# Optimization experiments

Hardware: AMD Instinct MI355X
Metric: run time of the kernel (lower is better)

Reference implementation:

```python
import jax, jax.numpy as jnp
import numpy as np

BN_EPS = 1e-5


def setup_inputs() -> dict:
    key = jax.random.key(0)
    ks = jax.random.split(key, 5)
    B, S, n_in, H, n_out = 256, 2048, 128, 256, 128
    return {
        "X": jax.random.normal(ks[0], (B, S, n_in), dtype=jnp.float32),
        "W_ih": jax.random.normal(ks[1], (H, n_in + H), dtype=jnp.float32) * (1.0 / np.sqrt(n_in + H)),
        "b_ih": jax.random.normal(ks[2], (H,), dtype=jnp.float32) * 0.02,
        "W_ho": jax.random.normal(ks[3], (n_out, H), dtype=jnp.float32) * (1.0 / np.sqrt(H)),
        "b_ho": jax.random.normal(ks[4], (n_out,), dtype=jnp.float32) * 0.02,
        "gamma": jnp.ones((H,), dtype=jnp.float32),
        "beta": jnp.zeros((H,), dtype=jnp.float32),
    }


def reference(X, W_ih, b_ih, W_ho, b_ho, gamma, beta):
    # X: (B, S, n_in). Recurrence over S with per-step training-mode BatchNorm1d
    # (batch statistics, biased variance, eps=1e-5), exact (erf) GELU.
    B = X.shape[0]
    H = W_ih.shape[0]
    Xt = jnp.transpose(X, (1, 0, 2))  # (S, B, n_in)

    def step(h, x):
        # combined: (B, n_in + H)
        z = jnp.concatenate([x, h], axis=-1) @ W_ih.T + b_ih  # (B, H)
        mu = jnp.mean(z, axis=0)
        var = jnp.var(z, axis=0)  # biased, matches torch BN training mode
        zn = (z - mu) * jax.lax.rsqrt(var + BN_EPS) * gamma + beta
        h_new = jax.nn.gelu(zn, approximate=False)
        o = jax.nn.gelu(h_new @ W_ho.T + b_ho, approximate=False)  # (B, n_out)
        return h_new, o

    h0 = jnp.zeros((B, H), dtype=X.dtype)
    _, outs = jax.lax.scan(step, h0, Xt)  # outs: (S, B, n_out)
    return jnp.transpose(outs, (1, 0, 2))  # (B, S, n_out)
```

## Files before the change

kernel.cpp:

```cpp
#include <hip/hip_runtime.h>
#include <stdint.h>


#define S_LEN 2048
#define BATCH 256
#define NIN   128
#define HID   256
#define NOUT  128

#define NBLK  128
#define NTHR  256
#define NR    16
#define NC    32
#define NO    16

#define HXW   392
#define WHOW  264

typedef short short8  __attribute__((ext_vector_type(8)));
typedef float float4v __attribute__((ext_vector_type(4)));

#define HXHI_OFF  0
#define HXLO_OFF  (16*HXW)
#define WHI_OFF   (2*16*HXW)
#define WLO_OFF   (2*16*HXW + 32*HXW)
#define WHOHI_OFF (2*16*HXW + 2*32*HXW)
#define WHOLO_OFF (WHOHI_OFF + 16*WHOW)
#define SHORTS_TOTAL (WHOLO_OFF + 16*WHOW)
#define RED_F 1088
#define SMEM_BYTES (SHORTS_TOTAL*2 + (2*RED_F + 256 + 256 + 16)*4)


#define MFMA(a,b,c) __builtin_amdgcn_mfma_f32_16x16x32_bf16(a,b,c,0,0,0)

#define AG_ST(p, v) __hip_atomic_store((p), (v), __ATOMIC_RELAXED, __HIP_MEMORY_SCOPE_AGENT)
#define AG_LD(p)    __hip_atomic_load((p), __ATOMIC_RELAXED, __HIP_MEMORY_SCOPE_AGENT)

__device__ __forceinline__ short f2bf(float f) {
  unsigned u = __float_as_uint(f);
  unsigned r = (u + 0x7fffu + ((u >> 16) & 1u)) >> 16;
  return (short)r;
}
__device__ __forceinline__ float bf2f(short s) {
  return __uint_as_float(((unsigned)(unsigned short)s) << 16);
}
__device__ __forceinline__ float gelu_f(float x) {
  return 0.5f * x * (1.0f + erff(x * 0.70710678118654752f));
}

__device__ __forceinline__ void stage_x(const float* __restrict__ X,
                                        short* hx_hi, short* hx_lo,
                                        int r0, int t, int tid) {
  int row = tid >> 4;
  int k0  = (tid & 15) * 8;
  const float* xp = X + ((size_t)(r0 + row) * S_LEN + t) * NIN + k0;
  float4v a = *(const float4v*)xp;
  float4v b = *(const float4v*)(xp + 4);
  short8 hi, lo;
#pragma unroll
  for (int j = 0; j < 4; ++j) {
    short h1 = f2bf(a[j]); hi[j] = h1; lo[j] = f2bf(a[j] - bf2f(h1));
  }
#pragma unroll
  for (int j = 0; j < 4; ++j) {
    short h1 = f2bf(b[j]); hi[4+j] = h1; lo[4+j] = f2bf(b[j] - bf2f(h1));
  }
  *(short8*)(hx_hi + row*HXW + k0) = hi;
  *(short8*)(hx_lo + row*HXW + k0) = lo;
}

__global__ void init_flags(unsigned* flags) {
  AG_ST(flags + (size_t)threadIdx.x * 32, 0u);
}

__global__ void __launch_bounds__(NTHR, 1)
rec_kernel(const float* __restrict__ X, const float* __restrict__ W_ih,
           const float* __restrict__ W_ho, const float* __restrict__ b_ho,
           const float* __restrict__ gamma, const float* __restrict__ beta,
           float* __restrict__ out, unsigned* __restrict__ flags,
           float* __restrict__ part, float* __restrict__ zbuf)
{
  extern __shared__ char smemraw[];
  short* sh      = (short*)smemraw;
  short* hx_hi   = sh + HXHI_OFF;
  short* hx_lo   = sh + HXLO_OFF;
  short* w_hi    = sh + WHI_OFF;
  short* w_lo    = sh + WLO_OFF;
  short* who_hi  = sh + WHOHI_OFF;
  short* who_lo  = sh + WHOLO_OFF;
  float* red     = (float*)(sh + SHORTS_TOTAL);
  float* red2    = red + RED_F;
  float* sscale  = red2 + RED_F;
  float* sshift  = sscale + 256;
  float* sbho    = sshift + 256;

  const int tid   = threadIdx.x;
  const int rowg  = blockIdx.x >> 3;
  const int colg  = blockIdx.x & 7;
  const int r0    = rowg * NR;
  const int c0    = colg * NC;
  const int oc0   = colg * NO;
  const int wv    = tid >> 6;
  const int lane  = tid & 63;
  const int nn    = lane & 15;
  const int quad  = lane >> 4;
  const int sub   = wv >> 1;
  const int khalf = wv & 1;

  for (int idx = tid; idx < NC * 384; idx += NTHR) {
    int r = idx / 384, j = idx % 384;
    float w = W_ih[(size_t)(c0 + r) * 384 + j];
    short hi = f2bf(w);
    w_hi[r*HXW + j] = hi;
    w_lo[r*HXW + j] = f2bf(w - bf2f(hi));
  }
  for (int idx = tid; idx < NO * 256; idx += NTHR) {
    int r = idx / 256, j = idx % 256;
    float w = W_ho[(size_t)(oc0 + r) * 256 + j];
    short hi = f2bf(w);
    who_hi[r*WHOW + j] = hi;
    who_lo[r*WHOW + j] = f2bf(w - bf2f(hi));
  }
  if (tid < NO) sbho[tid] = b_ho[oc0 + tid];
  for (int idx = tid; idx < 16 * 33; idx += NTHR) {
    int row = idx / 33, k0 = 128 + (idx % 33) * 8;
    short8 z8 = {0,0,0,0,0,0,0,0};
    *(short8*)(hx_hi + row*HXW + k0) = z8;
    *(short8*)(hx_lo + row*HXW + k0) = z8;
  }
  stage_x(X, hx_hi, hx_lo, r0, 0, tid);

  const float g_gamma = gamma[tid];
  const float g_beta  = beta[tid];
  __syncthreads();

  for (int t = 0; t < S_LEN; ++t) {
    const int p = t & 1;
    float* partp = part + p * (16 * 512);
    float* zbp   = zbuf + p * (BATCH * HID);

    float4v acc = {0.f, 0.f, 0.f, 0.f};
    {
      const short* arow_hi = hx_hi + nn*HXW;
      const short* arow_lo = hx_lo + nn*HXW;
      const short* brow_hi = w_hi + (sub*16 + nn)*HXW;
      const short* brow_lo = w_lo + (sub*16 + nn)*HXW;
      int kb = khalf*192 + quad*8;
#pragma unroll
      for (int ks = 0; ks < 6; ++ks) {
        short8 ah = *(const short8*)(arow_hi + kb);
        short8 al = *(const short8*)(arow_lo + kb);
        short8 bh = *(const short8*)(brow_hi + kb);
        short8 bl = *(const short8*)(brow_lo + kb);
        acc = MFMA(ah, bh, acc);
        acc = MFMA(ah, bl, acc);
        acc = MFMA(al, bh, acc);
        kb += 32;
      }
    }
    if (khalf == 1) {
#pragma unroll
      for (int i = 0; i < 4; ++i) red[sub*272 + (quad*4 + i)*17 + nn] = acc[i];
    }
    __syncthreads();
    if (khalf == 0) {
#pragma unroll
      for (int i = 0; i < 4; ++i) acc[i] += red[sub*272 + (quad*4 + i)*17 + nn];
      float* zb = zbp + (size_t)(r0 + quad*4) * HID + (c0 + sub*16 + nn);
#pragma unroll
      for (int i = 0; i < 4; ++i) AG_ST(zb + i*HID, acc[i]);
      float s = acc[0] + acc[1] + acc[2] + acc[3];
      float q = acc[0]*acc[0] + acc[1]*acc[1] + acc[2]*acc[2] + acc[3]*acc[3];
      s += __shfl_down(s, 32);  q += __shfl_down(q, 32);
      s += __shfl_down(s, 16);  q += __shfl_down(q, 16);
      if (lane < 16) {
        int c = c0 + sub*16 + lane;
        unsigned long long pv = ((unsigned long long)__float_as_uint(q) << 32)
                              | (unsigned long long)__float_as_uint(s);
        AG_ST((unsigned long long*)partp + (rowg*256 + c), pv);
      }
    }
    __syncthreads();

    if (tid == 0)
      AG_ST(flags + (size_t)blockIdx.x * 32, (unsigned)(t + 1));
    if (t + 1 < S_LEN) stage_x(X, hx_hi, hx_lo, r0, t + 1, tid);
    if (tid < NBLK) {
      const unsigned* fp = flags + (size_t)tid * 32;
      while (AG_LD(fp) < (unsigned)(t + 1)) __builtin_amdgcn_s_sleep(1);
    }
    __syncthreads();

    const int zrow = tid >> 4;
    const int zcb  = (tid & 15) * 16;
    unsigned long long zt[8];
    {
      const unsigned long long* zp = (const unsigned long long*)
          (zbp + (size_t)(r0 + zrow) * HID + zcb);
#pragma unroll
      for (int j = 0; j < 8; ++j) zt[j] = AG_LD(zp + j);
    }

    {
      const unsigned long long* pp = (const unsigned long long*)partp + tid;
      unsigned long long pv[16];
#pragma unroll
      for (int rg = 0; rg < 16; ++rg) pv[rg] = AG_LD(pp + rg*256);
      float sA = 0.f, sB = 0.f;
#pragma unroll
      for (int rg = 0; rg < 16; ++rg) {
        sA += __uint_as_float((unsigned)pv[rg]);
        sB += __uint_as_float((unsigned)(pv[rg] >> 32));
      }
      float mu   = sA * (1.0f/256.0f);
      float var  = sB * (1.0f/256.0f) - mu*mu;
      float rstd = rsqrtf(var + 1e-5f);
      float g    = g_gamma * rstd;
      sscale[tid] = g;
      sshift[tid] = g_beta - mu * g;
    }
    __syncthreads();

    {
      short hb[16], lb[16];
#pragma unroll
      for (int j = 0; j < 16; ++j) {
        float z  = __uint_as_float((unsigned)(zt[j >> 1] >> ((j & 1) * 32)));
        float zn = z * sscale[zcb + j] + sshift[zcb + j];
        float h  = gelu_f(zn);
        short hh = f2bf(h);
        hb[j] = hh; lb[j] = f2bf(h - bf2f(hh));
      }
      short* dh = hx_hi + zrow*HXW + 128 + zcb;
      short* dl = hx_lo + zrow*HXW + 128 + zcb;
      *(short8*)(dh)     = *(short8*)(hb);
      *(short8*)(dh + 8) = *(short8*)(hb + 8);
      *(short8*)(dl)     = *(short8*)(lb);
      *(short8*)(dl + 8) = *(short8*)(lb + 8);
    }
    __syncthreads();

    {
      float4v oacc = {0.f, 0.f, 0.f, 0.f};
      const short* arow_hi = hx_hi + nn*HXW + 128;
      const short* arow_lo = hx_lo + nn*HXW + 128;
      const short* brow_hi = who_hi + nn*WHOW;
      const short* brow_lo = who_lo + nn*WHOW;
      int kb = wv*64 + quad*8;
#pragma unroll
      for (int ks = 0; ks < 2; ++ks) {
        short8 ah = *(const short8*)(arow_hi + kb);
        short8 al = *(const short8*)(arow_lo + kb);
        short8 bh = *(const short8*)(brow_hi + kb);
        short8 bl = *(const short8*)(brow_lo + kb);
        oacc = MFMA(ah, bh, oacc);
        oacc = MFMA(ah, bl, oacc);
        oacc = MFMA(al, bh, oacc);
        kb += 32;
      }
#pragma unroll
      for (int i = 0; i < 4; ++i) red2[wv*272 + (quad*4 + i)*17 + nn] = oacc[i];
    }
    __syncthreads();
    {
      int row = tid >> 4, col = tid & 15;
      float v = red2[0*272 + row*17 + col] + red2[1*272 + row*17 + col]
              + red2[2*272 + row*17 + col] + red2[3*272 + row*17 + col]
              + sbho[col];
      out[((size_t)(r0 + row) * S_LEN + t) * NOUT + oc0 + col] = gelu_f(v);
    }
  }
}

extern "C" void kernel_launch(void* const* d_in, const int* in_sizes, int n_in,
                              void* d_out, int out_size, void* d_ws, size_t ws_size,
                              hipStream_t stream) {
  const float* X     = (const float*)d_in[0];
  const float* W_ih  = (const float*)d_in[1];
  const float* W_ho  = (const float*)d_in[3];
  const float* b_ho  = (const float*)d_in[4];
  const float* gamma = (const float*)d_in[5];
  const float* beta  = (const float*)d_in[6];
  float* out = (float*)d_out;

  unsigned* flags = (unsigned*)d_ws;
  float* part = (float*)((char*)d_ws + 16384);
  float* zbuf = part + 2 * 16 * 512;

  init_flags<<<dim3(1), dim3(NBLK), 0, stream>>>(flags);

  hipFuncSetAttribute((const void*)rec_kernel,
                      hipFuncAttributeMaxDynamicSharedMemorySize, SMEM_BYTES);

  rec_kernel<<<dim3(NBLK), dim3(NTHR), SMEM_BYTES, stream>>>(
      X, W_ih, W_ho, b_ho, gamma, beta, out, flags, part, zbuf);
}
```

Before: 13.36 ms.

## Replace flag barrier with tagged data polling and defer output GEMM

Replaces the per-step global flag barrier with step tags packed into each 64-bit z and partial-stat word, so consumers poll the data itself instead of all 128 block flags. The output projection for step t-1 is moved into the wait window of step t to hide its latency. This doubles the size of the z and stats buffers and their traffic, and adds a spin limit that could silently use stale data if it is ever hit.

```diff
diff --git a/kernel.cpp b/kernel.cpp
--- a/kernel.cpp
+++ b/kernel.cpp
@@ -17,8 +17,11 @@
 #define HXW   392
 #define WHOW  264
 
+#define SPIN_MAX (1u<<16)
+
 typedef short short8  __attribute__((ext_vector_type(8)));
 typedef float float4v __attribute__((ext_vector_type(4)));
+typedef unsigned long long u64;
 
 #define HXHI_OFF  0
 #define HXLO_OFF  (16*HXW)
@@ -30,11 +33,20 @@
 #define RED_F 1088
 #define SMEM_BYTES (SHORTS_TOTAL*2 + (2*RED_F + 256 + 256 + 16)*4)
 
+#define PART_U64 (2*16*256*2)
+#define ZBUF_U64 (2*BATCH*HID)
+#define WS_U64   (PART_U64 + ZBUF_U64)
 
 #define MFMA(a,b,c) __builtin_amdgcn_mfma_f32_16x16x32_bf16(a,b,c,0,0,0)
 
 #define AG_ST(p, v) __hip_atomic_store((p), (v), __ATOMIC_RELAXED, __HIP_MEMORY_SCOPE_AGENT)
 #define AG_LD(p)    __hip_atomic_load((p), __ATOMIC_RELAXED, __HIP_MEMORY_SCOPE_AGENT)
+
+__device__ __forceinline__ u64 packft(float f, unsigned tag) {
+  return (u64)__float_as_uint(f) | ((u64)tag << 32);
+}
+__device__ __forceinline__ float lo_f(u64 v) { return __uint_as_float((unsigned)v); }
+__device__ __forceinline__ unsigned hi_t(u64 v) { return (unsigned)(v >> 32); }
 
 __device__ __forceinline__ short f2bf(float f) {
   unsigned u = __float_as_uint(f);
@@ -69,16 +81,52 @@
   *(short8*)(hx_lo + row*HXW + k0) = lo;
 }
 
-__global__ void init_flags(unsigned* flags) {
-  AG_ST(flags + (size_t)threadIdx.x * 32, 0u);
+__device__ __forceinline__ void out_gemm_mfma(const short* hx_hi, const short* hx_lo,
+                                              const short* who_hi, const short* who_lo,
+                                              float* red2, int wv, int nn, int quad) {
+  float4v oacc = {0.f, 0.f, 0.f, 0.f};
+  const short* arow_hi = hx_hi + nn*HXW + 128;
+  const short* arow_lo = hx_lo + nn*HXW + 128;
+  const short* brow_hi = who_hi + nn*WHOW;
+  const short* brow_lo = who_lo + nn*WHOW;
+  int kb = wv*64 + quad*8;
+#pragma unroll
+  for (int ks = 0; ks < 2; ++ks) {
+    short8 ah = *(const short8*)(arow_hi + kb);
+    short8 al = *(const short8*)(arow_lo + kb);
+    short8 bh = *(const short8*)(brow_hi + kb);
+    short8 bl = *(const short8*)(brow_lo + kb);
+    oacc = MFMA(ah, bh, oacc);
+    oacc = MFMA(ah, bl, oacc);
+    oacc = MFMA(al, bh, oacc);
+    kb += 32;
+  }
+#pragma unroll
+  for (int i = 0; i < 4; ++i) red2[wv*272 + (quad*4 + i)*17 + nn] = oacc[i];
+}
+
+__device__ __forceinline__ void out_write(const float* red2, const float* sbho,
+                                          float* __restrict__ out,
+                                          int r0, int oc0, int t, int tid) {
+  int row = tid >> 4, col = tid & 15;
+  float v = red2[0*272 + row*17 + col] + red2[1*272 + row*17 + col]
+          + red2[2*272 + row*17 + col] + red2[3*272 + row*17 + col]
+          + sbho[col];
+  out[((size_t)(r0 + row) * S_LEN + t) * NOUT + oc0 + col] = gelu_f(v);
+}
+
+__global__ void init_tags(u64* ws) {
+  for (int i = blockIdx.x * blockDim.x + threadIdx.x; i < WS_U64;
+       i += gridDim.x * blockDim.x)
+    AG_ST(ws + i, 0ull);
 }
 
 __global__ void __launch_bounds__(NTHR, 1)
 rec_kernel(const float* __restrict__ X, const float* __restrict__ W_ih,
            const float* __restrict__ W_ho, const float* __restrict__ b_ho,
            const float* __restrict__ gamma, const float* __restrict__ beta,
-           float* __restrict__ out, unsigned* __restrict__ flags,
-           float* __restrict__ part, float* __restrict__ zbuf)
+           float* __restrict__ out,
+           u64* __restrict__ part, u64* __restrict__ zbuf)
 {
   extern __shared__ char smemraw[];
   short* sh      = (short*)smemraw;
@@ -134,10 +182,14 @@
   const float g_beta  = beta[tid];
   __syncthreads();
 
+  const int zrow = tid >> 4;
+  const int zcb  = (tid & 15) * 16;
+
   for (int t = 0; t < S_LEN; ++t) {
     const int p = t & 1;
-    float* partp = part + p * (16 * 512);
-    float* zbp   = zbuf + p * (BATCH * HID);
+    u64* partp = part + (size_t)p * (16*256*2);
+    u64* zbp   = zbuf + (size_t)p * (BATCH*HID);
+    const unsigned tag = (unsigned)(t + 1);
 
     float4v acc = {0.f, 0.f, 0.f, 0.f};
     {
@@ -166,52 +218,55 @@
     if (khalf == 0) {
 #pragma unroll
       for (int i = 0; i < 4; ++i) acc[i] += red[sub*272 + (quad*4 + i)*17 + nn];
-      float* zb = zbp + (size_t)(r0 + quad*4) * HID + (c0 + sub*16 + nn);
-#pragma unroll
-      for (int i = 0; i < 4; ++i) AG_ST(zb + i*HID, acc[i]);
+      u64* zb = zbp + (size_t)(r0 + quad*4) * HID + (c0 + sub*16 + nn);
+#pragma unroll
+      for (int i = 0; i < 4; ++i) AG_ST(zb + i*HID, packft(acc[i], tag));
       float s = acc[0] + acc[1] + acc[2] + acc[3];
       float q = acc[0]*acc[0] + acc[1]*acc[1] + acc[2]*acc[2] + acc[3]*acc[3];
       s += __shfl_down(s, 32);  q += __shfl_down(q, 32);
       s += __shfl_down(s, 16);  q += __shfl_down(q, 16);
       if (lane < 16) {
         int c = c0 + sub*16 + lane;
-        unsigned long long pv = ((unsigned long long)__float_as_uint(q) << 32)
-                              | (unsigned long long)__float_as_uint(s);
-        AG_ST((unsigned long long*)partp + (rowg*256 + c), pv);
-      }
-    }
-    __syncthreads();
-
-    if (tid == 0)
-      AG_ST(flags + (size_t)blockIdx.x * 32, (unsigned)(t + 1));
+        u64* pe = partp + ((size_t)rowg*256 + c)*2;
+        AG_ST(pe,     packft(s, tag));
+        AG_ST(pe + 1, packft(q, tag));
+      }
+    }
+    const u64* zp = zbp + (size_t)(r0 + zrow) * HID + zcb;
+    u64 zv[16], pv[16], qv[16];
+#pragma unroll
+    for (int j = 0; j < 16; ++j) zv[j] = AG_LD(zp + j);
+#pragma unroll
+    for (int rg = 0; rg < 16; ++rg) {
+      const u64* pe = partp + ((size_t)rg*256 + tid)*2;
+      pv[rg] = AG_LD(pe);
+      qv[rg] = AG_LD(pe + 1);
+    }
+
+    if (t > 0)
+      out_gemm_mfma(hx_hi, hx_lo, who_hi, who_lo, red2, wv, nn, quad);
+
     if (t + 1 < S_LEN) stage_x(X, hx_hi, hx_lo, r0, t + 1, tid);
-    if (tid < NBLK) {
-      const unsigned* fp = flags + (size_t)tid * 32;
-      while (AG_LD(fp) < (unsigned)(t + 1)) __builtin_amdgcn_s_sleep(1);
-    }
-    __syncthreads();
-
-    const int zrow = tid >> 4;
-    const int zcb  = (tid & 15) * 16;
-    unsigned long long zt[8];
-    {
-      const unsigned long long* zp = (const unsigned long long*)
-          (zbp + (size_t)(r0 + zrow) * HID + zcb);
-#pragma unroll
-      for (int j = 0; j < 8; ++j) zt[j] = AG_LD(zp + j);
-    }
-
-    {
-      const unsigned long long* pp = (const unsigned long long*)partp + tid;
-      unsigned long long pv[16];
-#pragma unroll
-      for (int rg = 0; rg < 16; ++rg) pv[rg] = AG_LD(pp + rg*256);
+
+    {
+      unsigned spin = 0;
+      for (;;) {
+        bool ok = true;
+#pragma unroll
+        for (int rg = 0; rg < 16; ++rg) {
+          const u64* pe = partp + ((size_t)rg*256 + tid)*2;
+          if (hi_t(pv[rg]) != tag) { ok = false; pv[rg] = AG_LD(pe); }
+          if (hi_t(qv[rg]) != tag) { ok = false; qv[rg] = AG_LD(pe + 1); }
+        }
+        if (ok || ++spin > SPIN_MAX) break;
+        __builtin_amdgcn_s_sleep(1);
+      }
+    }
+
+    {
       float sA = 0.f, sB = 0.f;
 #pragma unroll
-      for (int rg = 0; rg < 16; ++rg) {
-        sA += __uint_as_float((unsigned)pv[rg]);
-        sB += __uint_as_float((unsigned)(pv[rg] >> 32));
-      }
+      for (int rg = 0; rg < 16; ++rg) { sA += lo_f(pv[rg]); sB += lo_f(qv[rg]); }
       float mu   = sA * (1.0f/256.0f);
       float var  = sB * (1.0f/256.0f) - mu*mu;
       float rstd = rsqrtf(var + 1e-5f);
@@ -221,11 +276,25 @@
     }
     __syncthreads();
 
+    if (t > 0) out_write(red2, sbho, out, r0, oc0, t - 1, tid);
+
+    {
+      unsigned spin = 0;
+      for (;;) {
+        bool ok = true;
+#pragma unroll
+        for (int j = 0; j < 16; ++j)
+          if (hi_t(zv[j]) != tag) { ok = false; zv[j] = AG_LD(zp + j); }
+        if (ok || ++spin > SPIN_MAX) break;
+        __builtin_amdgcn_s_sleep(1);
+      }
+    }
+
     {
       short hb[16], lb[16];
 #pragma unroll
       for (int j = 0; j < 16; ++j) {
-        float z  = __uint_as_float((unsigned)(zt[j >> 1] >> ((j & 1) * 32)));
+        float z  = lo_f(zv[j]);
         float zn = z * sscale[zcb + j] + sshift[zcb + j];
         float h  = gelu_f(zn);
         short hh = f2bf(h);
@@ -240,36 +309,11 @@
     }
     __syncthreads();
 
-    {
-      float4v oacc = {0.f, 0.f, 0.f, 0.f};
-      const short* arow_hi = hx_hi + nn*HXW + 128;
-      const short* arow_lo = hx_lo + nn*HXW + 128;
-      const short* brow_hi = who_hi + nn*WHOW;
-      const short* brow_lo = who_lo + nn*WHOW;
-      int kb = wv*64 + quad*8;
-#pragma unroll
-      for (int ks = 0; ks < 2; ++ks) {
-        short8 ah = *(const short8*)(arow_hi + kb);
-        short8 al = *(const short8*)(arow_lo + kb);
-        short8 bh = *(const short8*)(brow_hi + kb);
-        short8 bl = *(const short8*)(brow_lo + kb);
-        oacc = MFMA(ah, bh, oacc);
-        oacc = MFMA(ah, bl, oacc);
-        oacc = MFMA(al, bh, oacc);
-        kb += 32;
-      }
-#pragma unroll
-      for (int i = 0; i < 4; ++i) red2[wv*272 + (quad*4 + i)*17 + nn] = oacc[i];
-    }
-    __syncthreads();
-    {
-      int row = tid >> 4, col = tid & 15;
-      float v = red2[0*272 + row*17 + col] + red2[1*272 + row*17 + col]
-              + red2[2*272 + row*17 + col] + red2[3*272 + row*17 + col]
-              + sbho[col];
-      out[((size_t)(r0 + row) * S_LEN + t) * NOUT + oc0 + col] = gelu_f(v);
-    }
-  }
+  }
+
+  out_gemm_mfma(hx_hi, hx_lo, who_hi, who_lo, red2, wv, nn, quad);
+  __syncthreads();
+  out_write(red2, sbho, out, r0, oc0, S_LEN - 1, tid);
 }
 
 extern "C" void kernel_launch(void* const* d_in, const int* in_sizes, int n_in,
@@ -283,15 +327,14 @@
   const float* beta  = (const float*)d_in[6];
   float* out = (float*)d_out;
 
-  unsigned* flags = (unsigned*)d_ws;
-  float* part = (float*)((char*)d_ws + 16384);
-  float* zbuf = part + 2 * 16 * 512;
-
-  init_flags<<<dim3(1), dim3(NBLK), 0, stream>>>(flags);
+  u64* part = (u64*)d_ws;
+  u64* zbuf = part + PART_U64;
+
+  init_tags<<<dim3(512), dim3(256), 0, stream>>>((u64*)d_ws);
 
   hipFuncSetAttribute((const void*)rec_kernel,
                       hipFuncAttributeMaxDynamicSharedMemorySize, SMEM_BYTES);
 
   rec_kernel<<<dim3(NBLK), dim3(NTHR), SMEM_BYTES, stream>>>(
-      X, W_ih, W_ho, b_ho, gamma, beta, out, flags, part, zbuf);
-}
+      X, W_ih, W_ho, b_ho, gamma, beta, out, part, zbuf);
+}
```

New measurement: 26.02 ms. 94.7% more time.

## Overlap deferred output GEMM with grid barrier wait and use per-wave flags

Applied to the files above, without the earlier changes.

The output projection for step t-1 now runs while the block waits at the cross-block barrier of step t, and its result is written after the next BN pass. The aim is to hide barrier latency and remove a block-wide sync before signalling. Each of the two producing waves raises its own flag right after its stores drain, and all 256 threads poll one flag each. The spin loop is capped at SPIN_MAX iterations, which could let a thread continue before data is ready. The z loads are also reordered to a strided column layout.

```diff
diff --git a/kernel.cpp b/kernel.cpp
--- a/kernel.cpp
+++ b/kernel.cpp
@@ -17,8 +17,12 @@
 #define HXW   392
 #define WHOW  264
 
+#define SPIN_MAX (1u<<16)
+
 typedef short short8  __attribute__((ext_vector_type(8)));
+typedef short short4v __attribute__((ext_vector_type(4)));
 typedef float float4v __attribute__((ext_vector_type(4)));
+typedef unsigned long long u64;
 
 #define HXHI_OFF  0
 #define HXLO_OFF  (16*HXW)
@@ -30,11 +34,19 @@
 #define RED_F 1088
 #define SMEM_BYTES (SHORTS_TOTAL*2 + (2*RED_F + 256 + 256 + 16)*4)
 
+#define FLAGS_U32 (256*32)
+#define PART_U64  (2*16*256)
 
 #define MFMA(a,b,c) __builtin_amdgcn_mfma_f32_16x16x32_bf16(a,b,c,0,0,0)
 
 #define AG_ST(p, v) __hip_atomic_store((p), (v), __ATOMIC_RELAXED, __HIP_MEMORY_SCOPE_AGENT)
 #define AG_LD(p)    __hip_atomic_load((p), __ATOMIC_RELAXED, __HIP_MEMORY_SCOPE_AGENT)
+
+__device__ __forceinline__ u64 pack2f(float s, float q) {
+  return (u64)__float_as_uint(s) | ((u64)__float_as_uint(q) << 32);
+}
+__device__ __forceinline__ float lo_f(u64 v) { return __uint_as_float((unsigned)v); }
+__device__ __forceinline__ float hi_f(u64 v) { return __uint_as_float((unsigned)(v >> 32)); }
 
 __device__ __forceinline__ short f2bf(float f) {
   unsigned u = __float_as_uint(f);
@@ -69,6 +81,40 @@
   *(short8*)(hx_lo + row*HXW + k0) = lo;
 }
 
+__device__ __forceinline__ void out_gemm_mfma(const short* hx_hi, const short* hx_lo,
+                                              const short* who_hi, const short* who_lo,
+                                              float* red2, int wv, int nn, int quad) {
+  float4v oacc = {0.f, 0.f, 0.f, 0.f};
+  const short* arow_hi = hx_hi + nn*HXW + 128;
+  const short* arow_lo = hx_lo + nn*HXW + 128;
+  const short* brow_hi = who_hi + nn*WHOW;
+  const short* brow_lo = who_lo + nn*WHOW;
+  int kb = wv*64 + quad*8;
+#pragma unroll
+  for (int ks = 0; ks < 2; ++ks) {
+    short8 ah = *(const short8*)(arow_hi + kb);
+    short8 al = *(const short8*)(arow_lo + kb);
+    short8 bh = *(const short8*)(brow_hi + kb);
+    short8 bl = *(const short8*)(brow_lo + kb);
+    oacc = MFMA(ah, bh, oacc);
+    oacc = MFMA(ah, bl, oacc);
+    oacc = MFMA(al, bh, oacc);
+    kb += 32;
+  }
+#pragma unroll
+  for (int i = 0; i < 4; ++i) red2[wv*272 + (quad*4 + i)*17 + nn] = oacc[i];
+}
+
+__device__ __forceinline__ void out_write(const float* red2, const float* sbho,
+                                          float* __restrict__ out,
+                                          int r0, int oc0, int t, int tid) {
+  int row = tid >> 4, col = tid & 15;
+  float v = red2[0*272 + row*17 + col] + red2[1*272 + row*17 + col]
+          + red2[2*272 + row*17 + col] + red2[3*272 + row*17 + col]
+          + sbho[col];
+  out[((size_t)(r0 + row) * S_LEN + t) * NOUT + oc0 + col] = gelu_f(v);
+}
+
 __global__ void init_flags(unsigned* flags) {
   AG_ST(flags + (size_t)threadIdx.x * 32, 0u);
 }
@@ -78,7 +124,7 @@
            const float* __restrict__ W_ho, const float* __restrict__ b_ho,
            const float* __restrict__ gamma, const float* __restrict__ beta,
            float* __restrict__ out, unsigned* __restrict__ flags,
-           float* __restrict__ part, float* __restrict__ zbuf)
+           u64* __restrict__ part, float* __restrict__ zbuf)
 {
   extern __shared__ char smemraw[];
   short* sh      = (short*)smemraw;
@@ -136,8 +182,9 @@
 
   for (int t = 0; t < S_LEN; ++t) {
     const int p = t & 1;
-    float* partp = part + p * (16 * 512);
-    float* zbp   = zbuf + p * (BATCH * HID);
+    u64*   partp = part + (size_t)p * (16*256);
+    float* zbp   = zbuf + (size_t)p * (BATCH*HID);
+    const unsigned tag = (unsigned)(t + 1);
 
     float4v acc = {0.f, 0.f, 0.f, 0.f};
     {
@@ -175,43 +222,41 @@
       s += __shfl_down(s, 16);  q += __shfl_down(q, 16);
       if (lane < 16) {
         int c = c0 + sub*16 + lane;
-        unsigned long long pv = ((unsigned long long)__float_as_uint(q) << 32)
-                              | (unsigned long long)__float_as_uint(s);
-        AG_ST((unsigned long long*)partp + (rowg*256 + c), pv);
+        AG_ST(partp + (size_t)rowg*256 + c, pack2f(s, q));
       }
+      asm volatile("s_waitcnt vmcnt(0)" ::: "memory");
+      if (lane == 0)
+        AG_ST(flags + ((size_t)blockIdx.x * 2 + sub) * 32, tag);
+    }
+
+    if (t > 0)
+      out_gemm_mfma(hx_hi, hx_lo, who_hi, who_lo, red2, wv, nn, quad);
+    if (t + 1 < S_LEN) stage_x(X, hx_hi, hx_lo, r0, t + 1, tid);
+
+    {
+      const unsigned* fp = flags + (size_t)tid * 32;
+      unsigned spin = 0;
+      while (AG_LD(fp) < tag && ++spin < SPIN_MAX)
+        __builtin_amdgcn_s_sleep(1);
     }
     __syncthreads();
 
-    if (tid == 0)
-      AG_ST(flags + (size_t)blockIdx.x * 32, (unsigned)(t + 1));
-    if (t + 1 < S_LEN) stage_x(X, hx_hi, hx_lo, r0, t + 1, tid);
-    if (tid < NBLK) {
-      const unsigned* fp = flags + (size_t)tid * 32;
-      while (AG_LD(fp) < (unsigned)(t + 1)) __builtin_amdgcn_s_sleep(1);
-    }
-    __syncthreads();
-
     const int zrow = tid >> 4;
-    const int zcb  = (tid & 15) * 16;
-    unsigned long long zt[8];
+    const int zcb  = (tid & 15) * 4;
+    u64 zt[4][2];
+#pragma unroll
+    for (int c4 = 0; c4 < 4; ++c4) {
+      const u64* zp = (const u64*)(zbp + (size_t)(r0 + zrow) * HID + zcb + c4*64);
+      zt[c4][0] = AG_LD(zp);
+      zt[c4][1] = AG_LD(zp + 1);
+    }
     {
-      const unsigned long long* zp = (const unsigned long long*)
-          (zbp + (size_t)(r0 + zrow) * HID + zcb);
-#pragma unroll
-      for (int j = 0; j < 8; ++j) zt[j] = AG_LD(zp + j);
-    }
-
-    {
-      const unsigned long long* pp = (const unsigned long long*)partp + tid;
-      unsigned long long pv[16];
-#pragma unroll
-      for (int rg = 0; rg < 16; ++rg) pv[rg] = AG_LD(pp + rg*256);
       float sA = 0.f, sB = 0.f;
-#pragma unroll
-      for (int rg = 0; rg < 16; ++rg) {
-        sA += __uint_as_float((unsigned)pv[rg]);
-        sB += __uint_as_float((unsigned)(pv[rg] >> 32));
-      }
+      u64 pv[16];
+#pragma unroll
+      for (int rg = 0; rg < 16; ++rg) pv[rg] = AG_LD(partp + (size_t)rg*256 + tid);
+#pragma unroll
+      for (int rg = 0; rg < 16; ++rg) { sA += lo_f(pv[rg]); sB += hi_f(pv[rg]); }
       float mu   = sA * (1.0f/256.0f);
       float var  = sB * (1.0f/256.0f) - mu*mu;
       float rstd = rsqrtf(var + 1e-5f);
@@ -222,54 +267,31 @@
     __syncthreads();
 
     {
-      short hb[16], lb[16];
-#pragma unroll
-      for (int j = 0; j < 16; ++j) {
-        float z  = __uint_as_float((unsigned)(zt[j >> 1] >> ((j & 1) * 32)));
-        float zn = z * sscale[zcb + j] + sshift[zcb + j];
-        float h  = gelu_f(zn);
-        short hh = f2bf(h);
-        hb[j] = hh; lb[j] = f2bf(h - bf2f(hh));
+#pragma unroll
+      for (int c4 = 0; c4 < 4; ++c4) {
+        int col = zcb + c4*64;
+        short4v h4, l4;
+#pragma unroll
+        for (int j = 0; j < 4; ++j) {
+          float z  = (j & 1) ? hi_f(zt[c4][j >> 1]) : lo_f(zt[c4][j >> 1]);
+          float zn = z * sscale[col + j] + sshift[col + j];
+          float h  = gelu_f(zn);
+          short hh = f2bf(h);
+          h4[j] = hh; l4[j] = f2bf(h - bf2f(hh));
+        }
+        *(short4v*)(hx_hi + zrow*HXW + 128 + col) = h4;
+        *(short4v*)(hx_lo + zrow*HXW + 128 + col) = l4;
       }
-      short* dh = hx_hi + zrow*HXW + 128 + zcb;
-      short* dl = hx_lo + zrow*HXW + 128 + zcb;
-      *(short8*)(dh)     = *(short8*)(hb);
-      *(short8*)(dh + 8) = *(short8*)(hb + 8);
-      *(short8*)(dl)     = *(short8*)(lb);
-      *(short8*)(dl + 8) = *(short8*)(lb + 8);
     }
     __syncthreads();
 
-    {
-      float4v oacc = {0.f, 0.f, 0.f, 0.f};
-      const short* arow_hi = hx_hi + nn*HXW + 128;
-      const short* arow_lo = hx_lo + nn*HXW + 128;
-      const short* brow_hi = who_hi + nn*WHOW;
-      const short* brow_lo = who_lo + nn*WHOW;
-      int kb = wv*64 + quad*8;
-#pragma unroll
-      for (int ks = 0; ks < 2; ++ks) {
-        short8 ah = *(const short8*)(arow_hi + kb);
-        short8 al = *(const short8*)(arow_lo + kb);
-        short8 bh = *(const short8*)(brow_hi + kb);
-        short8 bl = *(const short8*)(brow_lo + kb);
-        oacc = MFMA(ah, bh, oacc);
-        oacc = MFMA(ah, bl, oacc);
-        oacc = MFMA(al, bh, oacc);
-        kb += 32;
-      }
-#pragma unroll
-      for (int i = 0; i < 4; ++i) red2[wv*272 + (quad*4 + i)*17 + nn] = oacc[i];
-    }
-    __syncthreads();
-    {
-      int row = tid >> 4, col = tid & 15;
-      float v = red2[0*272 + row*17 + col] + red2[1*272 + row*17 + col]
-              + red2[2*272 + row*17 + col] + red2[3*272 + row*17 + col]
-              + sbho[col];
-      out[((size_t)(r0 + row) * S_LEN + t) * NOUT + oc0 + col] = gelu_f(v);
-    }
-  }
+    if (t > 0) out_write(red2, sbho, out, r0, oc0, t - 1, tid);
+  }
+
+  __syncthreads();
+  out_gemm_mfma(hx_hi, hx_lo, who_hi, who_lo, red2, wv, nn, quad);
+  __syncthreads();
+  out_write(red2, sbho, out, r0, oc0, S_LEN - 1, tid);
 }
 
 extern "C" void kernel_launch(void* const* d_in, const int* in_sizes, int n_in,
@@ -284,10 +306,10 @@
   float* out = (float*)d_out;
 
   unsigned* flags = (unsigned*)d_ws;
-  float* part = (float*)((char*)d_ws + 16384);
-  float* zbuf = part + 2 * 16 * 512;
-
-  init_flags<<<dim3(1), dim3(NBLK), 0, stream>>>(flags);
+  u64* part = (u64*)((char*)d_ws + FLAGS_U32*4);
+  float* zbuf = (float*)(part + PART_U64);
+
+  init_flags<<<dim3(1), dim3(256), 0, stream>>>(flags);
 
   hipFuncSetAttribute((const void*)rec_kernel,
                       hipFuncAttributeMaxDynamicSharedMemorySize, SMEM_BYTES);
```

Measured after the change: 12.98 ms. 2.8% less time.
